# Kernel tuning notes

Hardware: AMD Instinct MI355X
Metric: run time of the kernel (lower is better)

The kernel has to match this reference:

```python
import jax, jax.numpy as jnp
import numpy as np

BS, C_IN, S1 = 64, 256, 32
D_OUT, J = 32, 10          # out_dim, num_out_caps (as_final_output -> spatial_size_2)
I = S1 * S1                # num_in_caps = 1024
ROUTE_NUM = 3


def setup_inputs() -> dict:
    key = jax.random.key(0)
    k1, k2, k3 = jax.random.split(key, 3)
    x = jax.random.normal(k1, (BS, C_IN, S1, S1), dtype=jnp.float32)
    W = jax.random.normal(k2, (D_OUT * J, C_IN), dtype=jnp.float32) * 0.02  # 1x1 conv weight
    W_b = jax.random.normal(k3, (D_OUT * J,), dtype=jnp.float32) * 0.02     # conv bias
    return {"x": x, "W": W, "W_b": W_b}


def squash(vec):
    # vec: [bs, j, d]; coeff = ||v||^2 / (1+||v||^2) / ||v||
    norm = jnp.linalg.norm(vec, axis=2, keepdims=True)
    norm_sq = norm * norm
    return vec * (norm_sq / (1.0 + norm_sq) / norm)


def reference(x, W, W_b):
    bs = x.shape[0]
    # 1x1 conv == per-pixel matmul: [bs, J*D, h, w]
    pred = jnp.einsum('bchw,oc->bohw', x, W) + W_b[None, :, None, None]
    # torch: resize(bs, J, D, I) on contiguous tensor, then permute(0,3,1,2)
    pred = pred.reshape(bs, J, D_OUT, I).transpose(0, 3, 1, 2)  # [bs, I, J, D]
    b = jnp.zeros((bs, J, I), dtype=x.dtype)  # b_init='zero'
    v = None
    for _ in range(ROUTE_NUM):
        c = jax.nn.softmax(b, axis=1)                    # softmax over output caps j
        s = jnp.einsum('bji,bijd->bjd', c, pred)          # per-capsule weighted sum
        v = squash(s)                                     # [bs, J, D]
        delta_b = jnp.einsum('bjd,bijd->bji', v, pred)    # agreement
        b = b + jax.lax.stop_gradient(delta_b)            # torch .detach()
    return v  # as_final_output=True -> [bs, J, D]
```

## Files before the change

kernel.cpp:

```cpp
#include <hip/hip_runtime.h>
#include <hip/hip_bf16.h>

typedef __attribute__((ext_vector_type(8))) unsigned short u16x8;
typedef __attribute__((ext_vector_type(4))) unsigned short u16x4;
typedef __attribute__((ext_vector_type(8))) short short8;
typedef __attribute__((ext_vector_type(4))) float floatx4;

#define BS 64
#define CIN 256
#define II 1024
#define OO 320
#define JJ 10
#define DD 32

__device__ __forceinline__ float b2f(unsigned short u) {
    union { unsigned int i; float f; } x; x.i = ((unsigned int)u) << 16; return x.f;
}
__device__ __forceinline__ unsigned short f2b(float f) {
    union { float f; unsigned int i; } x; x.f = f;
    unsigned int r = x.i + 0x7fffu + ((x.i >> 16) & 1u);
    return (unsigned short)(r >> 16);
}
__device__ __forceinline__ float redlm(float v) {
    v += __shfl_xor(v, 1); v += __shfl_xor(v, 2);
    v += __shfl_xor(v, 4); v += __shfl_xor(v, 8);
    return v;
}

__global__ __launch_bounds__(256) void k_prepW(const float* __restrict__ W,
                                               unsigned short* __restrict__ Wl) {
    int gid = blockIdx.x * 256 + threadIdx.x;
    int lm = gid & 15;
    int quad = (gid >> 4) & 3;
    int mtl = (gid >> 6) & 3;
    int ks = (gid >> 8) & 7;
    int oc = gid >> 11;
    const float* src = W + (size_t)(oc * 64 + mtl * 16 + lm) * CIN + ks * 32 + quad * 8;
    float4 v0 = *(const float4*)src;
    float4 v1 = *(const float4*)(src + 4);
    u16x8 u;
    u[0] = f2b(v0.x); u[1] = f2b(v0.y); u[2] = f2b(v0.z); u[3] = f2b(v0.w);
    u[4] = f2b(v1.x); u[5] = f2b(v1.y); u[6] = f2b(v1.z); u[7] = f2b(v1.w);
    *(u16x8*)(Wl + (size_t)gid * 8) = u;
}

__global__ __launch_bounds__(512) void k_gemm3(const float* __restrict__ x,
                                               const unsigned short* __restrict__ Wl,
                                               const float* __restrict__ Wb,
                                               unsigned short* __restrict__ pred,
                                               float* __restrict__ psum0) {
    __shared__ unsigned short AsF[2048 * 8];
    __shared__ float ws_lds[8][OO];
    __shared__ float Wb_lds[OO];

    const int ic = blockIdx.x, b = blockIdx.y;
    const int t = threadIdx.x, w = t >> 6, l = t & 63;
    const int lm = l & 15, quad = l >> 4;

    if (t < OO) Wb_lds[t] = Wb[t];

    const float* xb = x + (size_t)b * CIN * II + ic * 128 + w * 16 + lm;
    short8 bfrag[8];
#pragma unroll
    for (int ks = 0; ks < 8; ++ks) {
        float tmp[8];
#pragma unroll
        for (int j = 0; j < 8; ++j) tmp[j] = xb[(size_t)(ks * 32 + quad * 8 + j) * II];
        short8 f;
#pragma unroll
        for (int j = 0; j < 8; ++j) f[j] = (short)f2b(tmp[j]);
        bfrag[ks] = f;
    }

    const int ibase = ic * 128 + w * 16 + lm;
#pragma unroll 1
    for (int oc = 0; oc < 5; ++oc) {
        __syncthreads();
        {
            const u16x8* src = (const u16x8*)Wl + oc * 2048;
            u16x8* dst = (u16x8*)AsF;
            for (int u = t; u < 2048; u += 512) dst[u] = src[u];
        }
        __syncthreads();

        floatx4 acc[4] = {};
#pragma unroll
        for (int ks = 0; ks < 8; ++ks)
#pragma unroll
            for (int mtl = 0; mtl < 4; ++mtl) {
                short8 af = *(const short8*)(AsF + (size_t)(((ks * 4 + mtl) * 4 + quad) * 16 + lm) * 8);
                acc[mtl] = __builtin_amdgcn_mfma_f32_16x16x32_bf16(af, bfrag[ks], acc[mtl], 0, 0, 0);
            }

#pragma unroll
        for (int mtl = 0; mtl < 4; ++mtl)
#pragma unroll
            for (int r = 0; r < 4; ++r) {
                int o = oc * 64 + mtl * 16 + quad * 4 + r;
                float v = acc[mtl][r] + Wb_lds[o];
                pred[((size_t)b * OO + o) * II + ibase] = f2b(v);
                float rs = redlm(v);
                if (lm == 0) ws_lds[w][o] = rs;
            }
    }
    __syncthreads();
    for (int u = t; u < OO; u += 512) {
        float s = 0.f;
#pragma unroll
        for (int ww = 0; ww < 8; ++ww) s += ws_lds[ww][u];
        psum0[((size_t)ic * BS + b) * OO + u] = s;
    }
}

template <bool FIRST>
__global__ __launch_bounds__(1024) void k_routeP(const float* __restrict__ psumIn, int nslice, float scale,
                                                 const unsigned short* __restrict__ pred,
                                                 float* __restrict__ blogG,
                                                 float* __restrict__ psumOut) {
    __shared__ float s_lds[OO];
    __shared__ float v_lds[OO];
    __shared__ float cf[JJ];
    __shared__ float dbuf[JJ][256];

    const int ic = blockIdx.x, b = blockIdx.y;
    const int t = threadIdx.x, w = t >> 6, l = t & 63;

    if (t < OO) {
        float s = 0.f;
        for (int sl = 0; sl < nslice; ++sl) s += psumIn[((size_t)sl * BS + b) * OO + t];
        s_lds[t] = scale * s;
    }
    __syncthreads();
    if (t < JJ) {
        float n2 = 0.f;
#pragma unroll
        for (int d = 0; d < DD; ++d) { float v = s_lds[t * DD + d]; n2 += v * v; }
        cf[t] = sqrtf(n2) / (1.0f + n2);
    }
    __syncthreads();
    if (t < OO) v_lds[t] = s_lds[t] * cf[t >> 5];
    __syncthreads();

    if (w < JJ) {
        float a0 = 0.f, a1 = 0.f, a2 = 0.f, a3 = 0.f;
        const unsigned short* rp = pred + ((size_t)b * OO + w * DD) * II + ic * 256 + l * 4;
#pragma unroll 8
        for (int d = 0; d < DD; ++d) {
            u16x4 u = *(const u16x4*)(rp + (size_t)d * II);
            float vv = v_lds[w * DD + d];
            a0 += vv * b2f(u[0]); a1 += vv * b2f(u[1]);
            a2 += vv * b2f(u[2]); a3 += vv * b2f(u[3]);
        }
        float4 lg;
        float* bg = blogG + ((size_t)b * JJ + w) * II + ic * 256 + l * 4;
        if (FIRST) {
            lg = make_float4(a0, a1, a2, a3);
            *(float4*)bg = lg;
        } else {
            float4 p = *(const float4*)bg;
            lg = make_float4(p.x + a0, p.y + a1, p.z + a2, p.w + a3);
        }
        *(float4*)&dbuf[w][l * 4] = lg;
    }
    __syncthreads();

    if (t < 256) {
        float lg[JJ];
#pragma unroll
        for (int j = 0; j < JJ; ++j) lg[j] = dbuf[j][t];
        float m = lg[0];
#pragma unroll
        for (int j = 1; j < JJ; ++j) m = fmaxf(m, lg[j]);
        float Z = 0.f, c[JJ];
#pragma unroll
        for (int j = 0; j < JJ; ++j) { c[j] = __expf(lg[j] - m); Z += c[j]; }
        float inv = 1.0f / Z;
#pragma unroll
        for (int j = 0; j < JJ; ++j) dbuf[j][t] = c[j] * inv;
    }
    __syncthreads();

    if (w < JJ) {
        float4 c4 = *(const float4*)&dbuf[w][l * 4];
        const unsigned short* rp = pred + ((size_t)b * OO + w * DD) * II + ic * 256 + l * 4;
#pragma unroll 4
        for (int d = 0; d < DD; ++d) {
            u16x4 u = *(const u16x4*)(rp + (size_t)d * II);
            float s = c4.x * b2f(u[0]) + c4.y * b2f(u[1]) + c4.z * b2f(u[2]) + c4.w * b2f(u[3]);
#pragma unroll
            for (int off = 32; off > 0; off >>= 1) s += __shfl_down(s, off);
            if (l == 0) psumOut[((size_t)ic * BS + b) * OO + w * DD + d] = s;
        }
    }
}

__global__ __launch_bounds__(320) void k_final2(const float* __restrict__ psum2,
                                                float* __restrict__ out) {
    __shared__ float s_lds[OO];
    __shared__ float cf[JJ];
    int b = blockIdx.x, t = threadIdx.x;
    float s = 0.f;
#pragma unroll
    for (int sl = 0; sl < 4; ++sl) s += psum2[((size_t)sl * BS + b) * OO + t];
    s_lds[t] = s;
    __syncthreads();
    if (t < JJ) {
        float n2 = 0.f;
#pragma unroll
        for (int d = 0; d < DD; ++d) { float v = s_lds[t * DD + d]; n2 += v * v; }
        cf[t] = sqrtf(n2) / (1.0f + n2);
    }
    __syncthreads();
    out[b * OO + t] = s_lds[t] * cf[t >> 5];
}

extern "C" void kernel_launch(void* const* d_in, const int* in_sizes, int n_in,
                              void* d_out, int out_size, void* d_ws, size_t ws_size,
                              hipStream_t stream) {
    const float* x  = (const float*)d_in[0];
    const float* W  = (const float*)d_in[1];
    const float* Wb = (const float*)d_in[2];

    char* ws = (char*)d_ws;
    unsigned short* pred = (unsigned short*)ws;
    unsigned short* Wl   = (unsigned short*)(ws + 41943040);
    float* psum0 = (float*)(ws + 42106880);
    float* psum1 = (float*)(ws + 42762240);
    float* psum2 = (float*)(ws + 43089920);
    float* blogG = (float*)(ws + 43417600);

    k_prepW<<<40, 256, 0, stream>>>(W, Wl);
    k_gemm3<<<dim3(8, BS), 512, 0, stream>>>(x, Wl, Wb, pred, psum0);
    k_routeP<true><<<dim3(4, BS), 1024, 0, stream>>>(psum0, 8, 0.1f, pred, blogG, psum1);
    k_routeP<false><<<dim3(4, BS), 1024, 0, stream>>>(psum1, 4, 1.0f, pred, blogG, psum2);
    k_final2<<<BS, 320, 0, stream>>>(psum2, (float*)d_out);
}
```

Before: 178.3 us.

## Stage GEMM output through LDS for coalesced stores; trim routing block size

The GEMM kernel now writes each 64-row output chunk into an LDS transpose buffer and then stores it to pred with 8-byte vector writes along the spatial dimension. Previously each lane wrote single 2-byte values scattered across rows. All x loads are issued up front into a register array before bf16 conversion, and launch bounds request two blocks per CU. The routing kernels drop from 1024 to 640 threads, so the 6 idle waves are gone. The cost is an extra barrier per oc iteration, more LDS use, and more register pressure from the 64-float staging array.

```diff
diff --git a/kernel.cpp b/kernel.cpp
--- a/kernel.cpp
+++ b/kernel.cpp
@@ -44,12 +44,13 @@
     *(u16x8*)(Wl + (size_t)gid * 8) = u;
 }
 
-__global__ __launch_bounds__(512) void k_gemm3(const float* __restrict__ x,
-                                               const unsigned short* __restrict__ Wl,
-                                               const float* __restrict__ Wb,
-                                               unsigned short* __restrict__ pred,
-                                               float* __restrict__ psum0) {
+__global__ __launch_bounds__(512, 2) void k_gemm3(const float* __restrict__ x,
+                                                  const unsigned short* __restrict__ Wl,
+                                                  const float* __restrict__ Wb,
+                                                  unsigned short* __restrict__ pred,
+                                                  float* __restrict__ psum0) {
     __shared__ unsigned short AsF[2048 * 8];
+    __shared__ unsigned short CT[64 * 132];
     __shared__ float ws_lds[8][OO];
     __shared__ float Wb_lds[OO];
 
@@ -60,19 +61,22 @@
     if (t < OO) Wb_lds[t] = Wb[t];
 
     const float* xb = x + (size_t)b * CIN * II + ic * 128 + w * 16 + lm;
+    float rx[64];
+#pragma unroll
+    for (int ks = 0; ks < 8; ++ks)
+#pragma unroll
+        for (int j = 0; j < 8; ++j)
+            rx[ks * 8 + j] = xb[(size_t)(ks * 32 + quad * 8 + j) * II];
+
     short8 bfrag[8];
 #pragma unroll
     for (int ks = 0; ks < 8; ++ks) {
-        float tmp[8];
-#pragma unroll
-        for (int j = 0; j < 8; ++j) tmp[j] = xb[(size_t)(ks * 32 + quad * 8 + j) * II];
         short8 f;
 #pragma unroll
-        for (int j = 0; j < 8; ++j) f[j] = (short)f2b(tmp[j]);
+        for (int j = 0; j < 8; ++j) f[j] = (short)f2b(rx[ks * 8 + j]);
         bfrag[ks] = f;
     }
 
-    const int ibase = ic * 128 + w * 16 + lm;
 #pragma unroll 1
     for (int oc = 0; oc < 5; ++oc) {
         __syncthreads();
@@ -96,12 +100,24 @@
         for (int mtl = 0; mtl < 4; ++mtl)
 #pragma unroll
             for (int r = 0; r < 4; ++r) {
-                int o = oc * 64 + mtl * 16 + quad * 4 + r;
-                float v = acc[mtl][r] + Wb_lds[o];
-                pred[((size_t)b * OO + o) * II + ibase] = f2b(v);
+                int o_l = mtl * 16 + quad * 4 + r;
+                float v = acc[mtl][r] + Wb_lds[oc * 64 + o_l];
+                CT[o_l * 132 + w * 16 + lm] = f2b(v);
                 float rs = redlm(v);
-                if (lm == 0) ws_lds[w][o] = rs;
+                if (lm == 0) ws_lds[w][oc * 64 + o_l] = rs;
             }
+        __syncthreads();
+
+        {
+            int r = t >> 5, col = (t & 31) * 4;
+            unsigned short* pbase = pred + ((size_t)b * OO + oc * 64) * II + ic * 128 + col;
+#pragma unroll
+            for (int p = 0; p < 4; ++p) {
+                int row = p * 16 + r;
+                u16x4 vv = *(const u16x4*)&CT[row * 132 + col];
+                *(u16x4*)(pbase + (size_t)row * II) = vv;
+            }
+        }
     }
     __syncthreads();
     for (int u = t; u < OO; u += 512) {
@@ -113,10 +129,10 @@
 }
 
 template <bool FIRST>
-__global__ __launch_bounds__(1024) void k_routeP(const float* __restrict__ psumIn, int nslice, float scale,
-                                                 const unsigned short* __restrict__ pred,
-                                                 float* __restrict__ blogG,
-                                                 float* __restrict__ psumOut) {
+__global__ __launch_bounds__(640) void k_routeP(const float* __restrict__ psumIn, int nslice, float scale,
+                                                const unsigned short* __restrict__ pred,
+                                                float* __restrict__ blogG,
+                                                float* __restrict__ psumOut) {
     __shared__ float s_lds[OO];
     __shared__ float v_lds[OO];
     __shared__ float cf[JJ];
@@ -141,7 +157,7 @@
     if (t < OO) v_lds[t] = s_lds[t] * cf[t >> 5];
     __syncthreads();
 
-    if (w < JJ) {
+    {
         float a0 = 0.f, a1 = 0.f, a2 = 0.f, a3 = 0.f;
         const unsigned short* rp = pred + ((size_t)b * OO + w * DD) * II + ic * 256 + l * 4;
 #pragma unroll 8
@@ -180,7 +196,7 @@
     }
     __syncthreads();
 
-    if (w < JJ) {
+    {
         float4 c4 = *(const float4*)&dbuf[w][l * 4];
         const unsigned short* rp = pred + ((size_t)b * OO + w * DD) * II + ic * 256 + l * 4;
 #pragma unroll 4
@@ -231,7 +247,7 @@
 
     k_prepW<<<40, 256, 0, stream>>>(W, Wl);
     k_gemm3<<<dim3(8, BS), 512, 0, stream>>>(x, Wl, Wb, pred, psum0);
-    k_routeP<true><<<dim3(4, BS), 1024, 0, stream>>>(psum0, 8, 0.1f, pred, blogG, psum1);
-    k_routeP<false><<<dim3(4, BS), 1024, 0, stream>>>(psum1, 4, 1.0f, pred, blogG, psum2);
+    k_routeP<true><<<dim3(4, BS), 640, 0, stream>>>(psum0, 8, 0.1f, pred, blogG, psum1);
+    k_routeP<false><<<dim3(4, BS), 640, 0, stream>>>(psum1, 4, 1.0f, pred, blogG, psum2);
     k_final2<<<BS, 320, 0, stream>>>(psum2, (float*)d_out);
 }
```

Measured after the change: 180.7 us. About the same (+1.3%).

## Fuse routing iterations into one cooperative kernel with register-resident pred

Applied to the files above, without the earlier changes.

Replaces the two routing kernels and the final squash kernel with a single cooperative kernel. Each block loads its slice of pred into registers once and reuses it across both routing passes, with grid.sync between passes for the cross-block sums. It also keeps the logits in registers instead of a global blog buffer and trims the block to 640 threads so only the 10 working waves run. In exchange it relies on all 256 blocks being co-resident for the cooperative launch, and the large per-thread register array may limit occupancy.

```diff
diff --git a/kernel.cpp b/kernel.cpp
--- a/kernel.cpp
+++ b/kernel.cpp
@@ -1,5 +1,8 @@
 #include <hip/hip_runtime.h>
+#include <hip/hip_cooperative_groups.h>
 #include <hip/hip_bf16.h>
+
+namespace cg = cooperative_groups;
 
 typedef __attribute__((ext_vector_type(8))) unsigned short u16x8;
 typedef __attribute__((ext_vector_type(4))) unsigned short u16x4;
@@ -24,6 +27,11 @@
 __device__ __forceinline__ float redlm(float v) {
     v += __shfl_xor(v, 1); v += __shfl_xor(v, 2);
     v += __shfl_xor(v, 4); v += __shfl_xor(v, 8);
+    return v;
+}
+__device__ __forceinline__ float redwave(float v) {
+    v += __shfl_xor(v, 1);  v += __shfl_xor(v, 2);  v += __shfl_xor(v, 4);
+    v += __shfl_xor(v, 8);  v += __shfl_xor(v, 16); v += __shfl_xor(v, 32);
     return v;
 }
 
@@ -112,11 +120,11 @@
     }
 }
 
-template <bool FIRST>
-__global__ __launch_bounds__(1024) void k_routeP(const float* __restrict__ psumIn, int nslice, float scale,
-                                                 const unsigned short* __restrict__ pred,
-                                                 float* __restrict__ blogG,
-                                                 float* __restrict__ psumOut) {
+__global__ __launch_bounds__(640, 3) void k_route_all3(const float* __restrict__ psum0,
+                                                       const unsigned short* __restrict__ pred,
+                                                       float* __restrict__ psum1,
+                                                       float* __restrict__ psum2,
+                                                       float* __restrict__ out) {
     __shared__ float s_lds[OO];
     __shared__ float v_lds[OO];
     __shared__ float cf[JJ];
@@ -124,94 +132,109 @@
 
     const int ic = blockIdx.x, b = blockIdx.y;
     const int t = threadIdx.x, w = t >> 6, l = t & 63;
+    cg::grid_group grid = cg::this_grid();
+
+    u16x4 vals[DD];
+    {
+        const unsigned short* pb = pred + ((size_t)b * OO + w * DD) * II + ic * 256 + 4 * l;
+#pragma unroll
+        for (int d = 0; d < DD; ++d)
+            vals[d] = *(const u16x4*)(pb + (size_t)d * II);
+    }
 
     if (t < OO) {
         float s = 0.f;
-        for (int sl = 0; sl < nslice; ++sl) s += psumIn[((size_t)sl * BS + b) * OO + t];
-        s_lds[t] = scale * s;
+#pragma unroll
+        for (int sl = 0; sl < 8; ++sl) s += psum0[((size_t)sl * BS + b) * OO + t];
+        s_lds[t] = 0.1f * s;
     }
     __syncthreads();
-    if (t < JJ) {
-        float n2 = 0.f;
-#pragma unroll
-        for (int d = 0; d < DD; ++d) { float v = s_lds[t * DD + d]; n2 += v * v; }
-        cf[t] = sqrtf(n2) / (1.0f + n2);
-    }
-    __syncthreads();
-    if (t < OO) v_lds[t] = s_lds[t] * cf[t >> 5];
-    __syncthreads();
-
-    if (w < JJ) {
-        float a0 = 0.f, a1 = 0.f, a2 = 0.f, a3 = 0.f;
-        const unsigned short* rp = pred + ((size_t)b * OO + w * DD) * II + ic * 256 + l * 4;
-#pragma unroll 8
+
+    float dl0 = 0.f, dl1 = 0.f, dl2 = 0.f, dl3 = 0.f;
+
+#pragma unroll 1
+    for (int pass = 0; pass < 2; ++pass) {
+        if (t < JJ) {
+            float n2 = 0.f;
+#pragma unroll
+            for (int d = 0; d < DD; ++d) { float v = s_lds[t * DD + d]; n2 += v * v; }
+            cf[t] = sqrtf(n2) / (1.0f + n2);
+        }
+        __syncthreads();
+        if (t < OO) v_lds[t] = s_lds[t] * cf[t >> 5];
+        __syncthreads();
+
+        float d0 = 0.f, d1 = 0.f, d2 = 0.f, d3 = 0.f;
+#pragma unroll
         for (int d = 0; d < DD; ++d) {
-            u16x4 u = *(const u16x4*)(rp + (size_t)d * II);
             float vv = v_lds[w * DD + d];
-            a0 += vv * b2f(u[0]); a1 += vv * b2f(u[1]);
-            a2 += vv * b2f(u[2]); a3 += vv * b2f(u[3]);
-        }
-        float4 lg;
-        float* bg = blogG + ((size_t)b * JJ + w) * II + ic * 256 + l * 4;
-        if (FIRST) {
-            lg = make_float4(a0, a1, a2, a3);
-            *(float4*)bg = lg;
+            d0 += vv * b2f(vals[d][0]);
+            d1 += vv * b2f(vals[d][1]);
+            d2 += vv * b2f(vals[d][2]);
+            d3 += vv * b2f(vals[d][3]);
+        }
+        float lg0, lg1, lg2, lg3;
+        if (pass == 0) {
+            dl0 = d0; dl1 = d1; dl2 = d2; dl3 = d3;
+            lg0 = d0; lg1 = d1; lg2 = d2; lg3 = d3;
         } else {
-            float4 p = *(const float4*)bg;
-            lg = make_float4(p.x + a0, p.y + a1, p.z + a2, p.w + a3);
-        }
-        *(float4*)&dbuf[w][l * 4] = lg;
-    }
-    __syncthreads();
-
-    if (t < 256) {
-        float lg[JJ];
-#pragma unroll
-        for (int j = 0; j < JJ; ++j) lg[j] = dbuf[j][t];
-        float m = lg[0];
-#pragma unroll
-        for (int j = 1; j < JJ; ++j) m = fmaxf(m, lg[j]);
-        float Z = 0.f, c[JJ];
-#pragma unroll
-        for (int j = 0; j < JJ; ++j) { c[j] = __expf(lg[j] - m); Z += c[j]; }
-        float inv = 1.0f / Z;
-#pragma unroll
-        for (int j = 0; j < JJ; ++j) dbuf[j][t] = c[j] * inv;
-    }
-    __syncthreads();
-
-    if (w < JJ) {
-        float4 c4 = *(const float4*)&dbuf[w][l * 4];
-        const unsigned short* rp = pred + ((size_t)b * OO + w * DD) * II + ic * 256 + l * 4;
-#pragma unroll 4
+            lg0 = dl0 + d0; lg1 = dl1 + d1; lg2 = dl2 + d2; lg3 = dl3 + d3;
+        }
+        dbuf[w][4 * l]     = lg0;
+        dbuf[w][4 * l + 1] = lg1;
+        dbuf[w][4 * l + 2] = lg2;
+        dbuf[w][4 * l + 3] = lg3;
+        __syncthreads();
+
+        if (t < 256) {
+            float lg[JJ];
+#pragma unroll
+            for (int j = 0; j < JJ; ++j) lg[j] = dbuf[j][t];
+            float m = lg[0];
+#pragma unroll
+            for (int j = 1; j < JJ; ++j) m = fmaxf(m, lg[j]);
+            float Z = 0.f, c[JJ];
+#pragma unroll
+            for (int j = 0; j < JJ; ++j) { c[j] = __expf(lg[j] - m); Z += c[j]; }
+            float inv = 1.0f / Z;
+#pragma unroll
+            for (int j = 0; j < JJ; ++j) dbuf[j][t] = c[j] * inv;
+        }
+        __syncthreads();
+
+        float c0 = dbuf[w][4 * l], c1 = dbuf[w][4 * l + 1];
+        float c2 = dbuf[w][4 * l + 2], c3 = dbuf[w][4 * l + 3];
+        float* pout = (pass == 0) ? psum1 : psum2;
+#pragma unroll
         for (int d = 0; d < DD; ++d) {
-            u16x4 u = *(const u16x4*)(rp + (size_t)d * II);
-            float s = c4.x * b2f(u[0]) + c4.y * b2f(u[1]) + c4.z * b2f(u[2]) + c4.w * b2f(u[3]);
-#pragma unroll
-            for (int off = 32; off > 0; off >>= 1) s += __shfl_down(s, off);
-            if (l == 0) psumOut[((size_t)ic * BS + b) * OO + w * DD + d] = s;
-        }
-    }
-}
-
-__global__ __launch_bounds__(320) void k_final2(const float* __restrict__ psum2,
-                                                float* __restrict__ out) {
-    __shared__ float s_lds[OO];
-    __shared__ float cf[JJ];
-    int b = blockIdx.x, t = threadIdx.x;
-    float s = 0.f;
-#pragma unroll
-    for (int sl = 0; sl < 4; ++sl) s += psum2[((size_t)sl * BS + b) * OO + t];
-    s_lds[t] = s;
-    __syncthreads();
-    if (t < JJ) {
-        float n2 = 0.f;
-#pragma unroll
-        for (int d = 0; d < DD; ++d) { float v = s_lds[t * DD + d]; n2 += v * v; }
-        cf[t] = sqrtf(n2) / (1.0f + n2);
-    }
-    __syncthreads();
-    out[b * OO + t] = s_lds[t] * cf[t >> 5];
+            float p = c0 * b2f(vals[d][0]) + c1 * b2f(vals[d][1])
+                    + c2 * b2f(vals[d][2]) + c3 * b2f(vals[d][3]);
+            p = redwave(p);
+            if (l == 0) pout[((size_t)ic * BS + b) * OO + w * DD + d] = p;
+        }
+        __syncthreads();
+        __threadfence();
+        grid.sync();
+
+        if (t < OO) {
+            float s = 0.f;
+#pragma unroll
+            for (int sl = 0; sl < 4; ++sl) s += pout[((size_t)sl * BS + b) * OO + t];
+            s_lds[t] = s;
+        }
+        __syncthreads();
+    }
+
+    if (ic == 0) {
+        if (t < JJ) {
+            float n2 = 0.f;
+#pragma unroll
+            for (int d = 0; d < DD; ++d) { float v = s_lds[t * DD + d]; n2 += v * v; }
+            cf[t] = sqrtf(n2) / (1.0f + n2);
+        }
+        __syncthreads();
+        if (t < OO) out[(size_t)b * OO + t] = s_lds[t] * cf[t >> 5];
+    }
 }
 
 extern "C" void kernel_launch(void* const* d_in, const int* in_sizes, int n_in,
@@ -227,11 +250,12 @@
     float* psum0 = (float*)(ws + 42106880);
     float* psum1 = (float*)(ws + 42762240);
     float* psum2 = (float*)(ws + 43089920);
-    float* blogG = (float*)(ws + 43417600);
+    float* out   = (float*)d_out;
 
     k_prepW<<<40, 256, 0, stream>>>(W, Wl);
     k_gemm3<<<dim3(8, BS), 512, 0, stream>>>(x, Wl, Wb, pred, psum0);
-    k_routeP<true><<<dim3(4, BS), 1024, 0, stream>>>(psum0, 8, 0.1f, pred, blogG, psum1);
-    k_routeP<false><<<dim3(4, BS), 1024, 0, stream>>>(psum1, 4, 1.0f, pred, blogG, psum2);
-    k_final2<<<BS, 320, 0, stream>>>(psum2, (float*)d_out);
-}
+
+    void* args[] = { (void*)&psum0, (void*)&pred, (void*)&psum1, (void*)&psum2, (void*)&out };
+    (void)hipLaunchCooperativeKernel((void*)k_route_all3, dim3(4, BS), dim3(640),
+                                     args, 0, stream);
+}
```

New measurement: 314.2 us. +76.2%, slower.
